# Performance work log

Hardware: AMD Instinct MI355X
Metric: run time of the kernel (lower is better)

Reference implementation:

```python
import jax, jax.numpy as jnp
import numpy as np

N = 50000          # nodes
E = 800000         # edges (COO)
IN_CH = 128
H1, H2, OUT = 200, 100, 2   # 100*out, 50*out, out with out_channels=2
EPS = 1e-12
DROP_P = 0.1


def setup_inputs() -> dict:
    key = jax.random.key(0)
    ks = jax.random.split(key, 6)
    x = jax.random.normal(ks[0], (N, IN_CH), dtype=jnp.float32)
    edge_index = jax.random.randint(ks[1], (2, E), 0, N)
    W1 = jax.random.normal(ks[2], (IN_CH, H1), dtype=jnp.float32) / np.sqrt(IN_CH)
    W2 = jax.random.normal(ks[3], (H1, H2), dtype=jnp.float32) / np.sqrt(H1)
    W3 = jax.random.normal(ks[4], (H2, OUT), dtype=jnp.float32) / np.sqrt(H2)
    beta1 = jnp.float32(1.0)
    beta2 = jnp.float32(1.0)
    beta3 = jnp.float32(1.0)
    return dict(x=x, edge_index=edge_index, W1=W1, W2=W2, W3=W3,
                beta1=beta1, beta2=beta2, beta3=beta3)


def _agnn_layer(x, W, beta, src, dst):
    # project in -> out channels, then AGNN cosine-attention propagation
    h = x @ W                                               # [N, D]
    hn = h / jnp.maximum(jnp.linalg.norm(h, axis=-1, keepdims=True), EPS)
    a = beta * jnp.sum(hn[src] * hn[dst], axis=-1)          # [E'] edge logits
    amax = jax.ops.segment_max(a, dst, num_segments=N)      # stable segment softmax
    amax = jnp.where(jnp.isfinite(amax), amax, 0.0)
    e = jnp.exp(a - amax[dst])
    denom = jax.ops.segment_sum(e, dst, num_segments=N)
    alpha = e / jnp.maximum(denom[dst], EPS)
    return jax.ops.segment_sum(h[src] * alpha[:, None], dst, num_segments=N)


def _dropout(k, x, p=DROP_P):
    keep = jax.random.bernoulli(k, 1.0 - p, x.shape)
    return jnp.where(keep, x / (1.0 - p), 0.0)


def reference(x, edge_index, W1, W2, W3, beta1, beta2, beta3):
    src, dst = edge_index[0], edge_index[1]
    loop = jnp.arange(N)                                    # self-loops (AGNNConv default)
    src = jnp.concatenate([src, loop])
    dst = jnp.concatenate([dst, loop])
    k1, k2 = jax.random.split(jax.random.key(42))
    h = jax.nn.relu(_agnn_layer(x, W1, beta1, src, dst))
    h = _dropout(k1, h)
    h = jax.nn.relu(_agnn_layer(h, W2, beta2, src, dst))
    h = _dropout(k2, h)
    h = jax.nn.relu(_agnn_layer(h, W3, beta3, src, dst))
    return h
```

## Files before the change

### kernel.cpp

```cpp
#include <hip/hip_runtime.h>
#include <hip/hip_bf16.h>

#define NN 50000
#define NE 800000
#define TE 850000
#define EPSN 1e-12f


#define H_OFF    0ull
#define A_OFF    40000000ull
#define H3_OFF   80000000ull
#define RINV_OFF 80400000ull
#define OFFS_OFF 80600000ull
#define DEG_OFF  80800016ull
#define CURS_OFF 81000016ull
#define ESRC_OFF 81200016ull
#define CHNK_OFF 84600016ull

__host__ __device__ inline void tf20(unsigned k0, unsigned k1, unsigned& x0, unsigned& x1) {
  unsigned ks2 = k0 ^ k1 ^ 0x1BD11BDAu;
  x0 += k0; x1 += k1;
#define TFR(r) { x0 += x1; x1 = ((x1 << (r)) | (x1 >> (32 - (r)))) ^ x0; }
  TFR(13) TFR(15) TFR(26) TFR(6)
  x0 += k1;  x1 += ks2 + 1u;
  TFR(17) TFR(29) TFR(16) TFR(24)
  x0 += ks2; x1 += k0 + 2u;
  TFR(13) TFR(15) TFR(26) TFR(6)
  x0 += k0;  x1 += k1 + 3u;
  TFR(17) TFR(29) TFR(16) TFR(24)
  x0 += k1;  x1 += ks2 + 4u;
  TFR(13) TFR(15) TFR(26) TFR(6)
  x0 += ks2; x1 += k0 + 5u;
#undef TFR
}

__device__ __forceinline__ float dropf(float val, unsigned k0, unsigned k1, unsigned i) {
  unsigned x0 = 0u, x1 = i;
  tf20(k0, k1, x0, x1);
  unsigned bits = x0 ^ x1;
  float u = __uint_as_float((bits >> 9) | 0x3F800000u) - 1.0f;
  return (u < 0.9f) ? val * (1.0f / 0.9f) : 0.0f;
}

__device__ __forceinline__ float wave_sum(float x) {
  x += __shfl_xor(x, 32); x += __shfl_xor(x, 16); x += __shfl_xor(x, 8);
  x += __shfl_xor(x, 4);  x += __shfl_xor(x, 2);  x += __shfl_xor(x, 1);
  return x;
}

__global__ __launch_bounds__(256) void csr_zero_kernel(int* __restrict__ p, int n) {
  int stride = gridDim.x * 256;
  for (int i = blockIdx.x * 256 + threadIdx.x; i < n; i += stride) p[i] = 0;
}

__global__ __launch_bounds__(256) void csr_hist_kernel(const int* __restrict__ ei, int* __restrict__ deg) {
  int e = blockIdx.x * 256 + threadIdx.x;
  if (e >= TE) return;
  int d = (e < NE) ? ei[NE + e] : (e - NE);
  atomicAdd(&deg[d], 1);
}

__global__ __launch_bounds__(256) void csr_scan1_kernel(const int* __restrict__ deg,
                                                        int* __restrict__ offs,
                                                        int* __restrict__ chunk) {
  __shared__ int lds[8];
  int t = threadIdx.x;
  int base = blockIdx.x * 1024 + t * 4;
  int d[4];
#pragma unroll
  for (int j = 0; j < 4; j++) d[j] = (base + j < NN) ? deg[base + j] : 0;
  int ts = d[0] + d[1] + d[2] + d[3];
  int lane = t & 63, wave = t >> 6;
  int inc = ts;
#pragma unroll
  for (int sh = 1; sh < 64; sh <<= 1) { int u = __shfl_up(inc, sh); if (lane >= sh) inc += u; }
  if (lane == 63) lds[wave] = inc;
  __syncthreads();
  if (t == 0) { int s = 0; for (int w = 0; w < 4; w++) { int x = lds[w]; lds[w] = s; s += x; } lds[4] = s; }
  __syncthreads();
  int p = lds[wave] + inc - ts;
#pragma unroll
  for (int j = 0; j < 4; j++) { if (base + j < NN) offs[base + j] = p; p += d[j]; }
  if (t == 255) chunk[blockIdx.x] = lds[4];
}

__global__ __launch_bounds__(64) void csr_scan2_kernel(int* __restrict__ chunk) {
  int t = threadIdx.x;
  int v = (t < 49) ? chunk[t] : 0;
  int inc = v;
#pragma unroll
  for (int sh = 1; sh < 64; sh <<= 1) { int u = __shfl_up(inc, sh); if (t >= sh) inc += u; }
  if (t < 49) chunk[t] = inc - v;
}

__global__ __launch_bounds__(256) void csr_scan3_kernel(int* __restrict__ offs,
                                                        const int* __restrict__ chunk,
                                                        int* __restrict__ curs) {
  int i = blockIdx.x * 256 + threadIdx.x;
  if (i < NN) {
    int val = offs[i] + chunk[i >> 10];
    offs[i] = val;
    curs[i] = val;
  }
  if (i == 0) offs[NN] = TE;
}

__global__ __launch_bounds__(256) void csr_scatter_kernel(const int* __restrict__ ei,
                                                          int* __restrict__ curs,
                                                          int* __restrict__ esrc) {
  int e = blockIdx.x * 256 + threadIdx.x;
  if (e >= TE) return;
  int s, d;
  if (e < NE) { s = ei[e]; d = ei[NE + e]; } else { s = d = e - NE; }
  int pos = atomicAdd(&curs[d], 1);
  esrc[pos] = s;
}

template<int K, int KT, int NLP, int N>
__device__ __forceinline__ void gemm_body(const float* __restrict__ A,
                                          const float* __restrict__ W,
                                          float* __restrict__ H,
                                          float* __restrict__ RINV, int M) {
  static_assert(NLP % 32 == 0, "NLP must be 32-granular");
  constexpr int KTP = KT + 1, NV = N / 4, NC = NLP / 32, CPT = NC * 4;
  __shared__ float As[64 * KTP];
  __shared__ float Ws[KT * NLP];
  const float4* A4 = (const float4*)A;
  const float4* W4 = (const float4*)W;
  const float4* Ws4 = (const float4*)Ws;

  int t = threadIdx.x, rgrp = t >> 3, cg = t & 7;
  int row0 = blockIdx.x * 64;
  float acc0[CPT], acc1[CPT];
#pragma unroll
  for (int j = 0; j < CPT; j++) { acc0[j] = 0.f; acc1[j] = 0.f; }

  for (int k0 = 0; k0 < K; k0 += KT) {
    __syncthreads();
    for (int idx = t; idx < 64 * (KT / 4); idx += 256) {
      int r = idx / (KT / 4), cq = idx - r * (KT / 4);
      int gr = row0 + r;
      float4 v = (gr < M) ? A4[(size_t)gr * (K / 4) + (k0 / 4) + cq]
                          : make_float4(0.f, 0.f, 0.f, 0.f);
      float* dst = &As[r * KTP + cq * 4];
      dst[0] = v.x; dst[1] = v.y; dst[2] = v.z; dst[3] = v.w;
    }
    for (int idx = t; idx < KT * NV; idx += 256) {
      int kk = idx / NV, cq = idx - kk * NV;
      *(float4*)&Ws[kk * NLP + cq * 4] = W4[(size_t)(k0 + kk) * NV + cq];
    }
    if (NLP > N) {
      for (int idx = t; idx < KT * ((NLP - N) / 4); idx += 256) {
        int kk = idx / ((NLP - N) / 4), cq = idx - kk * ((NLP - N) / 4);
        *(float4*)&Ws[kk * NLP + N + cq * 4] = make_float4(0.f, 0.f, 0.f, 0.f);
      }
    }
    __syncthreads();
#pragma unroll
    for (int kk = 0; kk < KT; kk++) {
      float a0 = As[(rgrp * 2) * KTP + kk];
      float a1 = As[(rgrp * 2 + 1) * KTP + kk];
#pragma unroll
      for (int q = 0; q < NC; q++) {
        float4 wv = Ws4[kk * (NLP / 4) + cg + 8 * q];
        acc0[q * 4 + 0] = fmaf(a0, wv.x, acc0[q * 4 + 0]);
        acc0[q * 4 + 1] = fmaf(a0, wv.y, acc0[q * 4 + 1]);
        acc0[q * 4 + 2] = fmaf(a0, wv.z, acc0[q * 4 + 2]);
        acc0[q * 4 + 3] = fmaf(a0, wv.w, acc0[q * 4 + 3]);
        acc1[q * 4 + 0] = fmaf(a1, wv.x, acc1[q * 4 + 0]);
        acc1[q * 4 + 1] = fmaf(a1, wv.y, acc1[q * 4 + 1]);
        acc1[q * 4 + 2] = fmaf(a1, wv.z, acc1[q * 4 + 2]);
        acc1[q * 4 + 3] = fmaf(a1, wv.w, acc1[q * 4 + 3]);
      }
    }
  }

  int r0 = row0 + rgrp * 2;
#pragma unroll
  for (int rr = 0; rr < 2; rr++) {
    int gr = r0 + rr;
    const float* acc = rr ? acc1 : acc0;
    float ss = 0.f;
#pragma unroll
    for (int q = 0; q < NC; q++) {
#pragma unroll
      for (int j = 0; j < 4; j++) {
        float v = acc[q * 4 + j];
        ss += v * v;
        int c = 4 * (cg + 8 * q) + j;
        if (gr < M && c < N) H[(size_t)gr * N + c] = v;
      }
    }
    ss += __shfl_xor(ss, 1); ss += __shfl_xor(ss, 2); ss += __shfl_xor(ss, 4);
    if (cg == 0 && gr < M) RINV[gr] = 1.0f / fmaxf(sqrtf(ss), EPSN);
  }
}

__global__ __launch_bounds__(256) void gemm1_kernel(const float* A, const float* W,
                                                    float* H, float* RINV, int M) {
  gemm_body<128, 32, 224, 200>(A, W, H, RINV, M);
}
__global__ __launch_bounds__(256) void gemm2_kernel(const float* A, const float* W,
                                                    float* H, float* RINV, int M) {
  gemm_body<200, 40, 128, 100>(A, W, H, RINV, M);
}

template<int D, int VEC, bool DROP>
__device__ __forceinline__ void attn_body(const float* __restrict__ H,
                                          const float* __restrict__ RINV,
                                          const int* __restrict__ OFFS,
                                          const int* __restrict__ ESRC,
                                          const float* __restrict__ BETA,
                                          float* __restrict__ OUT,
                                          unsigned k0, unsigned k1) {
  constexpr int NL = D / VEC;
  int v = blockIdx.x * 4 + (threadIdx.x >> 6);
  int lane = threadIdx.x & 63;
  bool act = lane < NL;
  const float* hrow = H + (size_t)v * D + lane * VEC;
  float hd[VEC];
#pragma unroll
  for (int j = 0; j < VEC; j++) hd[j] = 0.f;
  if (act) {
    if (VEC == 4) { float4 tv = *(const float4*)hrow; hd[0] = tv.x; hd[1] = tv.y; hd[2] = tv.z; hd[3] = tv.w; }
    else          { float2 tv = *(const float2*)hrow; hd[0] = tv.x; hd[1] = tv.y; }
  }
  float bd = BETA[0] * RINV[v];
  int e0 = OFFS[v], e1 = OFFS[v + 1];

  float s = 0.0f;
  float acc[VEC];
#pragma unroll
  for (int j = 0; j < VEC; j++) acc[j] = 0.0f;

  int idx = e0;
  for (; idx + 4 <= e1; idx += 4) {
    int   u[4];
    float r[4], dt[4], hs[4][VEC];
#pragma unroll
    for (int m = 0; m < 4; m++) u[m] = ESRC[idx + m];
#pragma unroll
    for (int m = 0; m < 4; m++) r[m] = RINV[u[m]];
#pragma unroll
    for (int m = 0; m < 4; m++) {
      const float* p = H + (size_t)u[m] * D + lane * VEC;
#pragma unroll
      for (int j = 0; j < VEC; j++) hs[m][j] = 0.f;
      if (act) {
        if (VEC == 4) { float4 a = *(const float4*)p; hs[m][0] = a.x; hs[m][1] = a.y; hs[m][2] = a.z; hs[m][3] = a.w; }
        else          { float2 a = *(const float2*)p; hs[m][0] = a.x; hs[m][1] = a.y; }
      }
    }
#pragma unroll
    for (int m = 0; m < 4; m++) {
      float d = 0.f;
#pragma unroll
      for (int j = 0; j < VEC; j++) d = fmaf(hd[j], hs[m][j], d);
      dt[m] = wave_sum(d);
    }
#pragma unroll
    for (int m = 0; m < 4; m++) {
      float w = __expf(bd * dt[m] * r[m]);
      s += w;
#pragma unroll
      for (int j = 0; j < VEC; j++) acc[j] = fmaf(w, hs[m][j], acc[j]);
    }
  }
  for (; idx < e1; ++idx) {
    int u0 = ESRC[idx];
    float r0 = RINV[u0];
    const float* p0 = H + (size_t)u0 * D + lane * VEC;
    float h0[VEC];
#pragma unroll
    for (int j = 0; j < VEC; j++) h0[j] = 0.f;
    if (act) {
      if (VEC == 4) { float4 a = *(const float4*)p0; h0[0] = a.x; h0[1] = a.y; h0[2] = a.z; h0[3] = a.w; }
      else          { float2 a = *(const float2*)p0; h0[0] = a.x; h0[1] = a.y; }
    }
    float d0 = 0.f;
#pragma unroll
    for (int j = 0; j < VEC; j++) d0 = fmaf(hd[j], h0[j], d0);
    d0 = wave_sum(d0);
    float w0 = __expf(bd * d0 * r0);
    s += w0;
#pragma unroll
    for (int j = 0; j < VEC; j++) acc[j] = fmaf(w0, h0[j], acc[j]);
  }

  float rs = 1.0f / fmaxf(s, EPSN);
  if (act) {
    float o[VEC];
#pragma unroll
    for (int j = 0; j < VEC; j++) {
      float val = acc[j] * rs;
      val = (val <= 0.0f) ? 0.0f : val;
      if (DROP) val = dropf(val, k0, k1, (unsigned)(v * D + lane * VEC + j));
      o[j] = val;
    }
    float* orow = OUT + (size_t)v * D + lane * VEC;
    if (VEC == 4) *(float4*)orow = make_float4(o[0], o[1], o[2], o[3]);
    else          *(float2*)orow = make_float2(o[0], o[1]);
  }
}

__global__ __launch_bounds__(256) void attn1_kernel(const float* H, const float* RINV,
                                                    const int* OFFS, const int* ESRC,
                                                    const float* BETA, float* OUT,
                                                    unsigned k0, unsigned k1) {
  attn_body<200, 4, true>(H, RINV, OFFS, ESRC, BETA, OUT, k0, k1);
}
__global__ __launch_bounds__(256) void attn2_kernel(const float* H, const float* RINV,
                                                    const int* OFFS, const int* ESRC,
                                                    const float* BETA, float* OUT,
                                                    unsigned k0, unsigned k1) {
  attn_body<100, 2, true>(H, RINV, OFFS, ESRC, BETA, OUT, k0, k1);
}

__global__ __launch_bounds__(256) void gemm3_kernel(const float* __restrict__ A2,
                                                    const float* __restrict__ W3,
                                                    float* __restrict__ H3,
                                                    float* __restrict__ RINV) {
  __shared__ float w3s[200];
  for (int i = threadIdx.x; i < 200; i += 256) w3s[i] = W3[i];
  __syncthreads();
  int v = blockIdx.x * 256 + threadIdx.x;
  if (v >= NN) return;
  const float* row = A2 + (size_t)v * 100;
  float o0 = 0.f, o1 = 0.f;
#pragma unroll 4
  for (int k = 0; k < 100; k++) {
    float x = row[k];
    o0 = fmaf(x, w3s[2 * k], o0);
    o1 = fmaf(x, w3s[2 * k + 1], o1);
  }
  H3[2 * v] = o0; H3[2 * v + 1] = o1;
  RINV[v] = 1.0f / fmaxf(sqrtf(o0 * o0 + o1 * o1), EPSN);
}

__global__ __launch_bounds__(256) void attn3_kernel(const float* __restrict__ H3,
                                                    const float* __restrict__ RINV,
                                                    const int* __restrict__ OFFS,
                                                    const int* __restrict__ ESRC,
                                                    const float* __restrict__ BETA,
                                                    float* __restrict__ out) {
  int v = blockIdx.x * 4 + (threadIdx.x >> 6);
  int lane = threadIdx.x & 63;
  float bd = BETA[0] * RINV[v];
  float h0 = H3[2 * v], h1 = H3[2 * v + 1];
  int e0 = OFFS[v], e1 = OFFS[v + 1];
  float s = 0.f, a0 = 0.f, a1 = 0.f;
  for (int idx = e0 + lane; idx < e1; idx += 64) {
    int u = ESRC[idx];
    float s0 = H3[2 * u], s1 = H3[2 * u + 1];
    float w = __expf(bd * (h0 * s0 + h1 * s1) * RINV[u]);
    s += w; a0 = fmaf(w, s0, a0); a1 = fmaf(w, s1, a1);
  }
  s = wave_sum(s); a0 = wave_sum(a0); a1 = wave_sum(a1);
  if (lane == 0) {
    float rs = 1.0f / fmaxf(s, EPSN);
    float o0 = a0 * rs, o1 = a1 * rs;
    out[2 * v]     = (o0 <= 0.0f) ? 0.0f : o0;
    out[2 * v + 1] = (o1 <= 0.0f) ? 0.0f : o1;
  }
}

extern "C" void kernel_launch(void* const* d_in, const int* in_sizes, int n_in,
                              void* d_out, int out_size, void* d_ws, size_t ws_size,
                              hipStream_t stream) {
  const float* X  = (const float*)d_in[0];
  const int*   EI = (const int*)d_in[1];
  const float* W1 = (const float*)d_in[2];
  const float* W2 = (const float*)d_in[3];
  const float* W3 = (const float*)d_in[4];
  const float* B1 = (const float*)d_in[5];
  const float* B2 = (const float*)d_in[6];
  const float* B3 = (const float*)d_in[7];

  char* ws = (char*)d_ws;
  float* H    = (float*)(ws + H_OFF);
  float* A    = (float*)(ws + A_OFF);
  float* H3   = (float*)(ws + H3_OFF);
  float* RINV = (float*)(ws + RINV_OFF);
  int* OFFS   = (int*)(ws + OFFS_OFF);
  int* DEG    = (int*)(ws + DEG_OFF);
  int* CURS   = (int*)(ws + CURS_OFF);
  int* ESRC   = (int*)(ws + ESRC_OFF);
  int* CHNK   = (int*)(ws + CHNK_OFF);

  unsigned k1a = 0u, k1b = 0u; tf20(0u, 42u, k1a, k1b);
  unsigned k2a = 0u, k2b = 1u; tf20(0u, 42u, k2a, k2b);

  csr_zero_kernel<<<64, 256, 0, stream>>>(DEG, NN);
  csr_hist_kernel<<<(TE + 255) / 256, 256, 0, stream>>>(EI, DEG);
  csr_scan1_kernel<<<49, 256, 0, stream>>>(DEG, OFFS, CHNK);
  csr_scan2_kernel<<<1, 64, 0, stream>>>(CHNK);
  csr_scan3_kernel<<<196, 256, 0, stream>>>(OFFS, CHNK, CURS);
  csr_scatter_kernel<<<(TE + 255) / 256, 256, 0, stream>>>(EI, CURS, ESRC);

  const int gb = (NN + 63) / 64;
  const int ab = NN / 4;

  gemm1_kernel<<<gb, 256, 0, stream>>>(X, W1, H, RINV, NN);
  attn1_kernel<<<ab, 256, 0, stream>>>(H, RINV, OFFS, ESRC, B1, A, k1a, k1b);
  gemm2_kernel<<<gb, 256, 0, stream>>>(A, W2, H, RINV, NN);
  attn2_kernel<<<ab, 256, 0, stream>>>(H, RINV, OFFS, ESRC, B2, A, k2a, k2b);
  gemm3_kernel<<<(NN + 255) / 256, 256, 0, stream>>>(A, W3, H3, RINV);
  attn3_kernel<<<ab, 256, 0, stream>>>(H3, RINV, OFFS, ESRC, B3, (float*)d_out);
}
```

Baseline: 514.5 us.

## Split each wave into two half-waves processing alternate edges in AGNN attention

The attention kernels now use each 64-lane wave as two 32-lane halves, each handling every other edge with a wider per-lane vector (8 floats for D=200, 4 for D=100). The partial softmax sums and accumulators are merged with a cross-half shuffle at the end, and an odd trailing edge is masked to one half. This aims to cut idle lanes (only 50 of 64 lanes were active before) and halve the serial edge-loop length, at the cost of more registers per lane. The degree-zeroing kernel is also replaced by hipMemsetAsync.

```diff
diff --git a/kernel.cpp b/kernel.cpp
--- a/kernel.cpp
+++ b/kernel.cpp
@@ -48,9 +48,10 @@
   return x;
 }
 
-__global__ __launch_bounds__(256) void csr_zero_kernel(int* __restrict__ p, int n) {
-  int stride = gridDim.x * 256;
-  for (int i = blockIdx.x * 256 + threadIdx.x; i < n; i += stride) p[i] = 0;
+__device__ __forceinline__ float half_sum(float x) {
+  x += __shfl_xor(x, 16); x += __shfl_xor(x, 8); x += __shfl_xor(x, 4);
+  x += __shfl_xor(x, 2);  x += __shfl_xor(x, 1);
+  return x;
 }
 
 __global__ __launch_bounds__(256) void csr_hist_kernel(const int* __restrict__ ei, int* __restrict__ deg) {
@@ -205,6 +206,22 @@
   gemm_body<200, 40, 128, 100>(A, W, H, RINV, M);
 }
 
+template<int VEC>
+__device__ __forceinline__ void loadrow(const float* __restrict__ p, float (&h)[VEC], bool act) {
+#pragma unroll
+  for (int j = 0; j < VEC; j++) h[j] = 0.f;
+  if (act) {
+    if (VEC == 8) {
+      float4 a = *(const float4*)p; float4 b = *(const float4*)(p + 4);
+      h[0] = a.x; h[1] = a.y; h[2] = a.z; h[3] = a.w;
+      h[4] = b.x; h[5] = b.y; h[6] = b.z; h[7] = b.w;
+    } else {
+      float4 a = *(const float4*)p;
+      h[0] = a.x; h[1] = a.y; h[2] = a.z; h[3] = a.w;
+    }
+  }
+}
+
 template<int D, int VEC, bool DROP>
 __device__ __forceinline__ void attn_body(const float* __restrict__ H,
                                           const float* __restrict__ RINV,
@@ -214,19 +231,17 @@
                                           float* __restrict__ OUT,
                                           unsigned k0, unsigned k1) {
   constexpr int NL = D / VEC;
+  static_assert(NL <= 32, "half-wave fragment");
   int v = blockIdx.x * 4 + (threadIdx.x >> 6);
   int lane = threadIdx.x & 63;
-  bool act = lane < NL;
-  const float* hrow = H + (size_t)v * D + lane * VEC;
+  int half = lane >> 5, sub = lane & 31;
+  bool act = sub < NL;
+
   float hd[VEC];
-#pragma unroll
-  for (int j = 0; j < VEC; j++) hd[j] = 0.f;
-  if (act) {
-    if (VEC == 4) { float4 tv = *(const float4*)hrow; hd[0] = tv.x; hd[1] = tv.y; hd[2] = tv.z; hd[3] = tv.w; }
-    else          { float2 tv = *(const float2*)hrow; hd[0] = tv.x; hd[1] = tv.y; }
-  }
+  loadrow<VEC>(H + (size_t)v * D + sub * VEC, hd, act);
   float bd = BETA[0] * RINV[v];
   int e0 = OFFS[v], e1 = OFFS[v + 1];
+  int npair2 = e0 + (((e1 - e0) >> 1) << 1);
 
   float s = 0.0f;
   float acc[VEC];
@@ -234,72 +249,78 @@
   for (int j = 0; j < VEC; j++) acc[j] = 0.0f;
 
   int idx = e0;
-  for (; idx + 4 <= e1; idx += 4) {
+  for (; idx + 8 <= npair2; idx += 8) {
     int   u[4];
-    float r[4], dt[4], hs[4][VEC];
-#pragma unroll
-    for (int m = 0; m < 4; m++) u[m] = ESRC[idx + m];
+    float r[4], hs[4][VEC];
+#pragma unroll
+    for (int m = 0; m < 4; m++) u[m] = ESRC[idx + 2 * m + half];
 #pragma unroll
     for (int m = 0; m < 4; m++) r[m] = RINV[u[m]];
 #pragma unroll
-    for (int m = 0; m < 4; m++) {
-      const float* p = H + (size_t)u[m] * D + lane * VEC;
-#pragma unroll
-      for (int j = 0; j < VEC; j++) hs[m][j] = 0.f;
-      if (act) {
-        if (VEC == 4) { float4 a = *(const float4*)p; hs[m][0] = a.x; hs[m][1] = a.y; hs[m][2] = a.z; hs[m][3] = a.w; }
-        else          { float2 a = *(const float2*)p; hs[m][0] = a.x; hs[m][1] = a.y; }
-      }
-    }
+    for (int m = 0; m < 4; m++)
+      loadrow<VEC>(H + (size_t)u[m] * D + sub * VEC, hs[m], act);
 #pragma unroll
     for (int m = 0; m < 4; m++) {
       float d = 0.f;
 #pragma unroll
       for (int j = 0; j < VEC; j++) d = fmaf(hd[j], hs[m][j], d);
-      dt[m] = wave_sum(d);
-    }
-#pragma unroll
-    for (int m = 0; m < 4; m++) {
-      float w = __expf(bd * dt[m] * r[m]);
+      float dt = half_sum(d);
+      float w = __expf(bd * dt * r[m]);
       s += w;
 #pragma unroll
       for (int j = 0; j < VEC; j++) acc[j] = fmaf(w, hs[m][j], acc[j]);
     }
   }
-  for (; idx < e1; ++idx) {
-    int u0 = ESRC[idx];
+  for (; idx < npair2; idx += 2) {
+    int u0 = ESRC[idx + half];
     float r0 = RINV[u0];
-    const float* p0 = H + (size_t)u0 * D + lane * VEC;
-    float h0[VEC];
-#pragma unroll
-    for (int j = 0; j < VEC; j++) h0[j] = 0.f;
-    if (act) {
-      if (VEC == 4) { float4 a = *(const float4*)p0; h0[0] = a.x; h0[1] = a.y; h0[2] = a.z; h0[3] = a.w; }
-      else          { float2 a = *(const float2*)p0; h0[0] = a.x; h0[1] = a.y; }
-    }
-    float d0 = 0.f;
-#pragma unroll
-    for (int j = 0; j < VEC; j++) d0 = fmaf(hd[j], h0[j], d0);
-    d0 = wave_sum(d0);
-    float w0 = __expf(bd * d0 * r0);
-    s += w0;
-#pragma unroll
-    for (int j = 0; j < VEC; j++) acc[j] = fmaf(w0, h0[j], acc[j]);
-  }
+    float hs0[VEC];
+    loadrow<VEC>(H + (size_t)u0 * D + sub * VEC, hs0, act);
+    float d = 0.f;
+#pragma unroll
+    for (int j = 0; j < VEC; j++) d = fmaf(hd[j], hs0[j], d);
+    float dt = half_sum(d);
+    float w = __expf(bd * dt * r0);
+    s += w;
+#pragma unroll
+    for (int j = 0; j < VEC; j++) acc[j] = fmaf(w, hs0[j], acc[j]);
+  }
+  if ((e1 - e0) & 1) {
+    int u0 = ESRC[e1 - 1];
+    float r0 = RINV[u0];
+    float hs0[VEC];
+    loadrow<VEC>(H + (size_t)u0 * D + sub * VEC, hs0, act);
+    float d = 0.f;
+#pragma unroll
+    for (int j = 0; j < VEC; j++) d = fmaf(hd[j], hs0[j], d);
+    float dt = half_sum(d);
+    float w = (half == 0) ? __expf(bd * dt * r0) : 0.0f;
+    s += w;
+#pragma unroll
+    for (int j = 0; j < VEC; j++) acc[j] = fmaf(w, hs0[j], acc[j]);
+  }
+
+  s += __shfl_xor(s, 32);
+#pragma unroll
+  for (int j = 0; j < VEC; j++) acc[j] += __shfl_xor(acc[j], 32);
 
   float rs = 1.0f / fmaxf(s, EPSN);
-  if (act) {
+  if (act && half == 0) {
     float o[VEC];
 #pragma unroll
     for (int j = 0; j < VEC; j++) {
       float val = acc[j] * rs;
       val = (val <= 0.0f) ? 0.0f : val;
-      if (DROP) val = dropf(val, k0, k1, (unsigned)(v * D + lane * VEC + j));
+      if (DROP) val = dropf(val, k0, k1, (unsigned)(v * D + sub * VEC + j));
       o[j] = val;
     }
-    float* orow = OUT + (size_t)v * D + lane * VEC;
-    if (VEC == 4) *(float4*)orow = make_float4(o[0], o[1], o[2], o[3]);
-    else          *(float2*)orow = make_float2(o[0], o[1]);
+    float* orow = OUT + (size_t)v * D + sub * VEC;
+    if (VEC == 8) {
+      *(float4*)orow = make_float4(o[0], o[1], o[2], o[3]);
+      *(float4*)(orow + 4) = make_float4(o[4], o[5], o[6], o[7]);
+    } else {
+      *(float4*)orow = make_float4(o[0], o[1], o[2], o[3]);
+    }
   }
 }
 
@@ -307,13 +328,13 @@
                                                     const int* OFFS, const int* ESRC,
                                                     const float* BETA, float* OUT,
                                                     unsigned k0, unsigned k1) {
-  attn_body<200, 4, true>(H, RINV, OFFS, ESRC, BETA, OUT, k0, k1);
+  attn_body<200, 8, true>(H, RINV, OFFS, ESRC, BETA, OUT, k0, k1);
 }
 __global__ __launch_bounds__(256) void attn2_kernel(const float* H, const float* RINV,
                                                     const int* OFFS, const int* ESRC,
                                                     const float* BETA, float* OUT,
                                                     unsigned k0, unsigned k1) {
-  attn_body<100, 2, true>(H, RINV, OFFS, ESRC, BETA, OUT, k0, k1);
+  attn_body<100, 4, true>(H, RINV, OFFS, ESRC, BETA, OUT, k0, k1);
 }
 
 __global__ __launch_bounds__(256) void gemm3_kernel(const float* __restrict__ A2,
@@ -390,7 +411,7 @@
   unsigned k1a = 0u, k1b = 0u; tf20(0u, 42u, k1a, k1b);
   unsigned k2a = 0u, k2b = 1u; tf20(0u, 42u, k2a, k2b);
 
-  csr_zero_kernel<<<64, 256, 0, stream>>>(DEG, NN);
+  hipMemsetAsync(DEG, 0, NN * sizeof(int), stream);
   csr_hist_kernel<<<(TE + 255) / 256, 256, 0, stream>>>(EI, DEG);
   csr_scan1_kernel<<<49, 256, 0, stream>>>(DEG, OFFS, CHNK);
   csr_scan2_kernel<<<1, 64, 0, stream>>>(CHNK);
```

Measured after the change: 511.6 us. Within noise of the previous version (-0.6%).
